# Optimization experiments

Hardware: AMD Instinct MI355X
Metric: run time of the kernel (lower is better)

The kernel has to match this reference:

```python
import jax, jax.numpy as jnp
import numpy as np

B, N_OBJ, OBJ_D = 256, 36, 2048
ATT_D, EMB_D, DEC_D, VOCAB, T = 1024, 1024, 1024, 10000, 20


def setup_inputs() -> dict:
    key = jax.random.key(0)
    ks = jax.random.split(key, 16)
    s = lambda *d: 1.0 / np.sqrt(d[-1])
    inp = {
        'encoder_out': jax.random.normal(ks[0], (B, EMB_D), jnp.float32),
        'objects': jax.random.normal(ks[1], (B, N_OBJ, OBJ_D), jnp.float32),
        'encoded_captions': jax.random.randint(ks[2], (B, T), 0, VOCAB),
        'caption_lengths': jax.random.randint(ks[3], (B, 1), 1, T + 1),
        'emb_table': jax.random.normal(ks[4], (VOCAB, EMB_D), jnp.float32) * 0.02,
        'W_enc_att': jax.random.normal(ks[5], (ATT_D, OBJ_D), jnp.float32) * s(OBJ_D),
        'b_enc_att': jnp.zeros((ATT_D,), jnp.float32),
        'W_dec_att': jax.random.normal(ks[6], (ATT_D, DEC_D), jnp.float32) * s(DEC_D),
        'b_dec_att': jnp.zeros((ATT_D,), jnp.float32),
        'w_full_att': jax.random.normal(ks[7], (1, ATT_D), jnp.float32) * s(ATT_D),
        'b_full_att': jnp.zeros((1,), jnp.float32),
        'W_fbeta': jax.random.normal(ks[8], (OBJ_D, DEC_D), jnp.float32) * s(DEC_D),
        'b_fbeta': jnp.zeros((OBJ_D,), jnp.float32),
        'W_ih': jax.random.normal(ks[9], (4 * DEC_D, EMB_D + OBJ_D), jnp.float32) * s(EMB_D + OBJ_D),
        'W_hh': jax.random.normal(ks[10], (4 * DEC_D, DEC_D), jnp.float32) * s(DEC_D),
        'b_ih': jnp.zeros((4 * DEC_D,), jnp.float32),
        'b_hh': jnp.zeros((4 * DEC_D,), jnp.float32),
        'W_fc': jax.random.normal(ks[11], (VOCAB, DEC_D), jnp.float32) * s(DEC_D),
        'b_fc': jnp.zeros((VOCAB,), jnp.float32),
    }
    return inp


def reference(encoder_out, objects, encoded_captions, caption_lengths,
              emb_table, W_enc_att, b_enc_att, W_dec_att, b_dec_att,
              w_full_att, b_full_att, W_fbeta, b_fbeta,
              W_ih, W_hh, b_ih, b_hh, W_fc, b_fc):
    lengths = caption_lengths[:, 0]
    sort_ind = jnp.argsort(-lengths)  # descending
    lengths = lengths[sort_ind]
    encoder_out = encoder_out[sort_ind]
    objects = objects[sort_ind]
    encoded_captions = encoded_captions[sort_ind]

    embeddings = emb_table[encoded_captions]  # (B, T, E)
    # step t input: encoder_out at t=0, embeddings[:, t-1] afterwards
    step_x = jnp.concatenate([encoder_out[:, None, :], embeddings[:, : T - 1, :]], axis=1)  # (B,T,E)

    att1 = jnp.einsum('bno,ao->bna', objects, W_enc_att) + b_enc_att  # (B,N,A), h-independent

    def step(carry, xs):
        h, c = carry
        x_t, t = xs  # (B,E), scalar
        active = (t < lengths)[:, None]  # (B,1) -- batch_size_t masking (lengths sorted desc)
        att2 = h @ W_dec_att.T + b_dec_att  # (B,A)
        e = (jax.nn.relu(att1 + att2[:, None, :]) @ w_full_att[0] + b_full_att[0])  # (B,N)
        alpha = jax.nn.softmax(e, axis=1)
        awe = jnp.einsum('bn,bno->bo', alpha, objects)  # (B,O)
        gate = jax.nn.sigmoid(h @ W_fbeta.T + b_fbeta)
        awe = gate * awe
        gates = jnp.concatenate([x_t, awe], axis=-1) @ W_ih.T + b_ih + h @ W_hh.T + b_hh
        i, f, g, o = jnp.split(gates, 4, axis=-1)  # torch LSTMCell order
        c_new = jax.nn.sigmoid(f) * c + jax.nn.sigmoid(i) * jnp.tanh(g)
        h_new = jax.nn.sigmoid(o) * jnp.tanh(c_new)
        h = jnp.where(active, h_new, h)
        c = jnp.where(active, c_new, c)
        preds = h_new @ W_fc.T + b_fc  # dropout in eval mode = identity
        preds = jnp.where(active, preds, 0.0)
        alpha = jnp.where(active, alpha, 0.0)
        return (h, c), (preds, alpha)

    h0 = jnp.zeros((B, DEC_D), objects.dtype)
    c0 = jnp.zeros((B, DEC_D), objects.dtype)
    xs = (jnp.swapaxes(step_x, 0, 1), jnp.arange(T))
    _, (preds, alphas) = jax.lax.scan(step, (h0, c0), xs)
    predictions = jnp.swapaxes(preds, 0, 1)  # (B,T,V)
    alphas = jnp.swapaxes(alphas, 0, 1)      # (B,T,N)
    return predictions, encoded_captions, lengths, alphas, sort_ind
```

## Files before the change

### kernel.cpp

```cpp
#include <hip/hip_runtime.h>
#include <hip/hip_bf16.h>
#include <cstdint>
#include <cstddef>

#define BB 256
#define TT 20
#define NOBJ 36
#define OBJD 2048
#define ATTD 1024
#define DECD 1024
#define VOCAB 10000
#define NBIG  17168
#define NBIGP 17216
#define NSPLIT 7168

typedef unsigned short u16;
typedef __attribute__((ext_vector_type(8))) short short8v;
typedef __attribute__((ext_vector_type(4))) float float4v;

__device__ inline u16 f2bf(float f) {
    __hip_bfloat16 h = __float2bfloat16(f);
    return *reinterpret_cast<u16*>(&h);
}
__device__ inline float bu(u16 u) {
    union { unsigned int i; float f; } x;
    x.i = ((unsigned int)u) << 16;
    return x.f;
}
__device__ inline float sigf(float x) { return 1.f / (1.f + expf(-x)); }

__global__ __launch_bounds__(256) void sort_kernel(
    const int* __restrict__ lens, int* __restrict__ sidx, int* __restrict__ slen,
    int* __restrict__ cnt, float* __restrict__ out_len, float* __restrict__ out_sind)
{
    __shared__ int L[BB];
    __shared__ int SL[BB];
    const int i = threadIdx.x;
    const int li = lens[i];
    L[i] = li;
    __syncthreads();
    int r = 0;
    for (int j = 0; j < BB; ++j) {
        const int lj = L[j];
        if (lj > li || (lj == li && j < i)) r++;
    }
    sidx[r] = i;
    slen[r] = li;
    SL[r] = li;
    out_sind[r] = (float)i;
    out_len[r]  = (float)li;
    __syncthreads();
    if (i < TT) {
        int cc = 0;
        for (int b = 0; b < BB; ++b) cc += (SL[b] > i);
        cnt[i] = cc;
    }
}

__global__ __launch_bounds__(256) void meta_kernel(
    const int* __restrict__ caps, const int* __restrict__ sidx,
    float* __restrict__ out_caps)
{
    const int idx = blockIdx.x * 256 + threadIdx.x;
    const int p = idx / TT, t = idx % TT;
    out_caps[idx] = (float)caps[sidx[p] * TT + t];
}

__global__ __launch_bounds__(256) void gather_objs(
    const float* __restrict__ objs, const int* __restrict__ sidx,
    u16* __restrict__ objsb)
{
    const int row = blockIdx.x;
    const int b = row / NOBJ, n = row - b * NOBJ;
    const float* src = objs + ((size_t)sidx[b] * NOBJ + n) * OBJD;
    u16* dst = objsb + (size_t)row * OBJD;
    const int tid = threadIdx.x;
    #pragma unroll
    for (int j = 0; j < 2; ++j) {
        float4 v = ((const float4*)src)[tid + 256 * j];
        ushort4 s;
        s.x = f2bf(v.x); s.y = f2bf(v.y); s.z = f2bf(v.z); s.w = f2bf(v.w);
        ((ushort4*)dst)[tid + 256 * j] = s;
    }
}

__global__ __launch_bounds__(256) void convWbig(
    const float* __restrict__ Wda, const float* __restrict__ bda,
    const float* __restrict__ Wfb, const float* __restrict__ bfb,
    const float* __restrict__ Whh,
    const float* __restrict__ Wfc, const float* __restrict__ bfc,
    u16* __restrict__ Wb, float* __restrict__ bcat)
{
    const int n = blockIdx.x;
    const int tid = threadIdx.x;
    const float* src = nullptr;
    float bb = 0.f;
    if (n < 1024)        { src = Wda + (size_t)n * 1024;            bb = bda[n]; }
    else if (n < 3072)   { src = Wfb + (size_t)(n - 1024) * 1024;   bb = bfb[n - 1024]; }
    else if (n < 7168)   { src = Whh + (size_t)(n - 3072) * 1024;   bb = 0.f; }
    else if (n < NBIG)   { src = Wfc + (size_t)(n - 7168) * 1024;   bb = bfc[n - 7168]; }
    u16* dst = Wb + (size_t)n * 1024;
    ushort4 s;
    if (src) {
        float4 v = ((const float4*)src)[tid];
        s.x = f2bf(v.x); s.y = f2bf(v.y); s.z = f2bf(v.z); s.w = f2bf(v.w);
    } else { s.x = s.y = s.z = s.w = 0; }
    ((ushort4*)dst)[tid] = s;
    if (tid == 0) bcat[n] = bb;
}

__global__ __launch_bounds__(256) void convWih(
    const float* __restrict__ Wih, const float* __restrict__ bih,
    const float* __restrict__ bhh, u16* __restrict__ Wb, float* __restrict__ bsum)
{
    const int n = blockIdx.x;
    const int tid = threadIdx.x;
    const float* src = Wih + (size_t)n * 3072;
    u16* dst = Wb + (size_t)n * 3072;
    #pragma unroll
    for (int j = 0; j < 3; ++j) {
        float4 v = ((const float4*)src)[tid + 256 * j];
        ushort4 s;
        s.x = f2bf(v.x); s.y = f2bf(v.y); s.z = f2bf(v.z); s.w = f2bf(v.w);
        ((ushort4*)dst)[tid + 256 * j] = s;
    }
    if (tid == 0) bsum[n] = bih[n] + bhh[n];
}

__global__ __launch_bounds__(256) void convWea(
    const float* __restrict__ Wea, u16* __restrict__ Wb)
{
    const int n = blockIdx.x;
    const int tid = threadIdx.x;
    const float* src = Wea + (size_t)n * OBJD;
    u16* dst = Wb + (size_t)n * OBJD;
    #pragma unroll
    for (int j = 0; j < 2; ++j) {
        float4 v = ((const float4*)src)[tid + 256 * j];
        ushort4 s;
        s.x = f2bf(v.x); s.y = f2bf(v.y); s.z = f2bf(v.z); s.w = f2bf(v.w);
        ((ushort4*)dst)[tid + 256 * j] = s;
    }
}

__global__ __launch_bounds__(256) void embed_kernel(
    const float* __restrict__ enc, const int* __restrict__ caps,
    const float* __restrict__ emb, const int* __restrict__ sidx,
    u16* __restrict__ Xb)
{
    const int blk = blockIdx.x;
    const int t = blk >> 8;
    const int b = blk & 255;
    const int sb = sidx[b];
    const float* src = (t == 0) ? (enc + (size_t)sb * DECD)
                                : (emb + (size_t)caps[sb * TT + (t - 1)] * DECD);
    const int tid = threadIdx.x;
    float4 v = ((const float4*)src)[tid];
    ushort4 s;
    s.x = f2bf(v.x); s.y = f2bf(v.y); s.z = f2bf(v.z); s.w = f2bf(v.w);
    ((ushort4*)(Xb + (size_t)blk * DECD))[tid] = s;
}

__global__ __launch_bounds__(256) void zero_hc(float* __restrict__ h, float* __restrict__ c)
{
    const int idx = blockIdx.x * 256 + threadIdx.x;
    if (idx < BB * DECD) h[idx] = 0.f;
    else                 c[idx - BB * DECD] = 0.f;
}

__global__ __launch_bounds__(256) void hcat0_kernel(
    const float* __restrict__ bcat, float* __restrict__ Hcat)
{
    const int col4 = blockIdx.x * 256 + threadIdx.x;
    const int m = blockIdx.y;
    ((float4*)(Hcat + (size_t)m * 7168))[col4] = ((const float4*)bcat)[col4];
}

template<int MF>
__global__ __launch_bounds__(256) void gemm_mfma(
    const u16* __restrict__ A, int lda,
    const u16* __restrict__ B, int ldb,
    const float* __restrict__ bias,
    float* __restrict__ C, u16* __restrict__ Cb, int ldc,
    int Nreal, int K,
    int nsplit, float* __restrict__ C2, int ldc2, const int* __restrict__ cntp)
{
    constexpr int BM = 64 * MF;
    constexpr int BK = 32;
    __shared__ u16 As[BM * BK];
    __shared__ u16 Bs[64 * BK];
    const int tid = threadIdx.x;
    const int lane = tid & 63;
    const int w = tid >> 6;
    const int m0 = blockIdx.y * BM;
    const int n0 = blockIdx.x * 64;

    float4v acc[MF][4];
    #pragma unroll
    for (int i = 0; i < MF; ++i)
        #pragma unroll
        for (int j = 0; j < 4; ++j) acc[i][j] = (float4v){0.f, 0.f, 0.f, 0.f};

    const int pa = tid * MF;
    const int ra = pa >> 2;
    const int fa = (ra >> 1) & 3;
    const int rb = tid >> 2;
    const int cbs = (tid & 3) ^ ((rb >> 1) & 3);
    const u16* Arow = A + (size_t)(m0 + ra) * lda;
    const u16* Brow = B + (size_t)(n0 + rb) * ldb;

    const int cfrag = lane >> 4;
    int slotA[MF], slotB[4];
    #pragma unroll
    for (int mi = 0; mi < MF; ++mi) {
        const int r = w * (16 * MF) + mi * 16 + (lane & 15);
        slotA[mi] = 4 * r + (cfrag ^ ((r >> 1) & 3));
    }
    #pragma unroll
    for (int nj = 0; nj < 4; ++nj) {
        const int rn = nj * 16 + (lane & 15);
        slotB[nj] = 4 * rn + (cfrag ^ ((rn >> 1) & 3));
    }

    for (int k0 = 0; k0 < K; k0 += BK) {
        short8v ast[MF];
        #pragma unroll
        for (int s = 0; s < MF; ++s) {
            const int c = ((pa + s) & 3) ^ fa;
            ast[s] = *(const short8v*)(Arow + k0 + c * 8);
        }
        short8v bst = *(const short8v*)(Brow + k0 + cbs * 8);
        __syncthreads();
        #pragma unroll
        for (int s = 0; s < MF; ++s)
            *(short8v*)&As[(pa + s) * 8] = ast[s];
        *(short8v*)&Bs[tid * 8] = bst;
        __syncthreads();

        short8v av[MF], bv[4];
        #pragma unroll
        for (int mi = 0; mi < MF; ++mi) av[mi] = *(const short8v*)&As[slotA[mi] * 8];
        #pragma unroll
        for (int nj = 0; nj < 4; ++nj) bv[nj] = *(const short8v*)&Bs[slotB[nj] * 8];
        #pragma unroll
        for (int mi = 0; mi < MF; ++mi)
            #pragma unroll
            for (int nj = 0; nj < 4; ++nj)
                acc[mi][nj] = __builtin_amdgcn_mfma_f32_16x16x32_bf16(
                    av[mi], bv[nj], acc[mi][nj], 0, 0, 0);
    }

    const int act = cntp ? *cntp : (1 << 30);
    #pragma unroll
    for (int mi = 0; mi < MF; ++mi) {
        const int mbase = m0 + w * (16 * MF) + mi * 16 + ((lane >> 4) << 2);
        #pragma unroll
        for (int nj = 0; nj < 4; ++nj) {
            const int n = n0 + nj * 16 + (lane & 15);
            if (n >= Nreal) continue;
            const float bval = bias[n];
            #pragma unroll
            for (int r = 0; r < 4; ++r) {
                const int m = mbase + r;
                const float v = acc[mi][nj][r] + bval;
                if (n < nsplit) {
                    if (Cb) Cb[(size_t)m * ldc + n] = f2bf(v);
                    else    C [(size_t)m * ldc + n] = v;
                } else {
                    C2[(size_t)m * ldc2 + (n - nsplit)] = (m < act) ? v : 0.f;
                }
            }
        }
    }
}

__global__ __launch_bounds__(256) void attn_kernel(
    const u16* __restrict__ att1b, const float* __restrict__ Hcat,
    const u16* __restrict__ objsb,
    const float* __restrict__ wfa, const float* __restrict__ bfa,
    const u16* __restrict__ Xb,
    const int* __restrict__ slen, int t,
    float* __restrict__ out_alph, u16* __restrict__ xcatb)
{
    __shared__ float wred[4][40];
    __shared__ float es[40];
    __shared__ float alph[40];
    const int b = blockIdx.x, tid = threadIdx.x;
    const int lane = tid & 63, w = tid >> 6;
    const float* hrow = Hcat + (size_t)b * 7168;
    const float4 h4 = ((const float4*)hrow)[tid];
    const float4 w4 = ((const float4*)wfa)[tid];
    const u16* a1base = att1b + (size_t)b * NOBJ * ATTD;

    float ep[NOBJ];
    #pragma unroll
    for (int n = 0; n < NOBJ; ++n) {
        ushort4 a4 = ((const ushort4*)(a1base + (size_t)n * ATTD))[tid];
        const float v0 = fmaxf(bu(a4.x) + h4.x, 0.f);
        const float v1 = fmaxf(bu(a4.y) + h4.y, 0.f);
        const float v2 = fmaxf(bu(a4.z) + h4.z, 0.f);
        const float v3 = fmaxf(bu(a4.w) + h4.w, 0.f);
        ep[n] = v0 * w4.x + v1 * w4.y + v2 * w4.z + v3 * w4.w;
    }
    #pragma unroll
    for (int n = 0; n < NOBJ; ++n) {
        float p = ep[n];
        #pragma unroll
        for (int off = 32; off > 0; off >>= 1) p += __shfl_down(p, off, 64);
        if (lane == 0) wred[w][n] = p;
    }
    __syncthreads();
    if (tid < NOBJ)
        es[tid] = wred[0][tid] + wred[1][tid] + wred[2][tid] + wred[3][tid] + bfa[0];
    __syncthreads();
    if (tid == 0) {
        float m = es[0];
        for (int n = 1; n < NOBJ; ++n) m = fmaxf(m, es[n]);
        float s = 0.f;
        for (int n = 0; n < NOBJ; ++n) { const float e = expf(es[n] - m); alph[n] = e; s += e; }
        const float inv = 1.f / s;
        for (int n = 0; n < NOBJ; ++n) alph[n] *= inv;
    }
    __syncthreads();
    const bool active = t < slen[b];
    if (tid < NOBJ)
        out_alph[((size_t)b * TT + t) * NOBJ + tid] = active ? alph[tid] : 0.f;

    float acc[8] = {0.f, 0.f, 0.f, 0.f, 0.f, 0.f, 0.f, 0.f};
    const u16* ob = objsb + (size_t)b * NOBJ * OBJD + tid * 8;
    #pragma unroll 4
    for (int n = 0; n < NOBJ; ++n) {
        const short8v ov = *(const short8v*)(ob + (size_t)n * OBJD);
        const float al = alph[n];
        #pragma unroll
        for (int j = 0; j < 8; ++j) acc[j] = fmaf(al, bu((u16)ov[j]), acc[j]);
    }
    const float* gp = hrow + 1024 + tid * 8;
    const float4 g0 = *(const float4*)gp;
    const float4 g1 = *(const float4*)(gp + 4);
    float gt[8] = {sigf(g0.x), sigf(g0.y), sigf(g0.z), sigf(g0.w),
                   sigf(g1.x), sigf(g1.y), sigf(g1.z), sigf(g1.w)};
    short8v st;
    #pragma unroll
    for (int j = 0; j < 8; ++j) st[j] = (short)f2bf(acc[j] * gt[j]);
    *(short8v*)&xcatb[(size_t)b * 3072 + 1024 + tid * 8] = st;

    ((ushort4*)(xcatb + (size_t)b * 3072))[tid] =
        ((const ushort4*)(Xb + ((size_t)t * BB + b) * DECD))[tid];
}

__global__ __launch_bounds__(256) void lstm_kernel(
    const float* __restrict__ G2, const float* __restrict__ Hcat,
    float* __restrict__ h, float* __restrict__ c, u16* __restrict__ hb,
    const int* __restrict__ slen, int t)
{
    const int idx = blockIdx.x * 256 + threadIdx.x;
    const int b = idx >> 8, d4 = idx & 255;
    const float4* g2 = (const float4*)(G2 + (size_t)b * 4096);
    const float4* hw = (const float4*)(Hcat + (size_t)b * 7168 + 3072);
    const float4 vi = g2[d4],       wi = hw[d4];
    const float4 vf = g2[256 + d4], wf = hw[256 + d4];
    const float4 vg = g2[512 + d4], wg = hw[512 + d4];
    const float4 vo = g2[768 + d4], wo = hw[768 + d4];
    float4* hp = (float4*)(h + (size_t)b * 1024);
    float4* cp = (float4*)(c + (size_t)b * 1024);
    const float4 hold = hp[d4];
    const float4 cold = cp[d4];
    float4 cn, hn;
    {
        const float si = sigf(vi.x + wi.x), sf = sigf(vf.x + wf.x), so = sigf(vo.x + wo.x);
        cn.x = sf * cold.x + si * tanhf(vg.x + wg.x); hn.x = so * tanhf(cn.x);
    }
    {
        const float si = sigf(vi.y + wi.y), sf = sigf(vf.y + wf.y), so = sigf(vo.y + wo.y);
        cn.y = sf * cold.y + si * tanhf(vg.y + wg.y); hn.y = so * tanhf(cn.y);
    }
    {
        const float si = sigf(vi.z + wi.z), sf = sigf(vf.z + wf.z), so = sigf(vo.z + wo.z);
        cn.z = sf * cold.z + si * tanhf(vg.z + wg.z); hn.z = so * tanhf(cn.z);
    }
    {
        const float si = sigf(vi.w + wi.w), sf = sigf(vf.w + wf.w), so = sigf(vo.w + wo.w);
        cn.w = sf * cold.w + si * tanhf(vg.w + wg.w); hn.w = so * tanhf(cn.w);
    }
    const bool active = t < slen[b];
    const float4 hcur = active ? hn : hold;
    if (active) { hp[d4] = hn; cp[d4] = cn; }
    ushort4 s;
    s.x = f2bf(hcur.x); s.y = f2bf(hcur.y); s.z = f2bf(hcur.z); s.w = f2bf(hcur.w);
    ((ushort4*)(hb + (size_t)b * 1024))[d4] = s;
}

extern "C" void kernel_launch(void* const* d_in, const int* in_sizes, int n_in,
                              void* d_out, int out_size, void* d_ws, size_t ws_size,
                              hipStream_t stream)
{
    const float* enc  = (const float*)d_in[0];
    const float* objs = (const float*)d_in[1];
    const int*   caps = (const int*)d_in[2];
    const int*   clen = (const int*)d_in[3];
    const float* emb  = (const float*)d_in[4];
    const float* Wea  = (const float*)d_in[5];
    const float* bea  = (const float*)d_in[6];
    const float* Wda  = (const float*)d_in[7];
    const float* bda  = (const float*)d_in[8];
    const float* wfa  = (const float*)d_in[9];
    const float* bfa  = (const float*)d_in[10];
    const float* Wfb  = (const float*)d_in[11];
    const float* bfb  = (const float*)d_in[12];
    const float* Wih  = (const float*)d_in[13];
    const float* Whh  = (const float*)d_in[14];
    const float* bih  = (const float*)d_in[15];
    const float* bhh  = (const float*)d_in[16];
    const float* Wfc  = (const float*)d_in[17];
    const float* bfc  = (const float*)d_in[18];

    float* outP     = (float*)d_out;
    float* out_caps = outP + (size_t)BB * TT * VOCAB;
    float* out_len  = out_caps + BB * TT;
    float* out_alph = out_len + BB;
    float* out_sind = out_alph + (size_t)BB * TT * NOBJ;

    char* wp = (char*)d_ws;
    auto alloc = [&](size_t bytes) -> void* {
        void* r = (void*)wp;
        wp += (bytes + 255) & ~(size_t)255;
        return r;
    };
    int*   sidx  = (int*)alloc(BB * 4);
    int*   slen  = (int*)alloc(BB * 4);
    int*   cnt   = (int*)alloc(32 * 4);
    u16*   objsb = (u16*)alloc((size_t)BB * NOBJ * OBJD * 2);
    u16*   Wbigb = (u16*)alloc((size_t)NBIGP * 1024 * 2);
    float* bcat  = (float*)alloc(NBIGP * 4);
    u16*   Wihb  = (u16*)alloc((size_t)4096 * 3072 * 2);
    float* bsum  = (float*)alloc(4096 * 4);
    u16*   Weab  = (u16*)alloc((size_t)1024 * OBJD * 2);
    u16*   att1b = (u16*)alloc((size_t)BB * NOBJ * ATTD * 2);
    u16*   Xb    = (u16*)alloc((size_t)TT * BB * DECD * 2);
    float* Hcat  = (float*)alloc((size_t)BB * 7168 * 4);
    u16*   xcatb = (u16*)alloc((size_t)BB * 3072 * 2);
    float* G2    = (float*)alloc((size_t)BB * 4096 * 4);
    float* h     = (float*)alloc((size_t)BB * DECD * 4);
    float* c     = (float*)alloc((size_t)BB * DECD * 4);
    u16*   hb    = (u16*)alloc((size_t)BB * DECD * 2);
    (void)ws_size; (void)in_sizes; (void)n_in; (void)out_size;

    sort_kernel<<<1, 256, 0, stream>>>(clen, sidx, slen, cnt, out_len, out_sind);
    meta_kernel<<<20, 256, 0, stream>>>(caps, sidx, out_caps);
    gather_objs<<<BB * NOBJ, 256, 0, stream>>>(objs, sidx, objsb);
    convWbig<<<NBIGP, 256, 0, stream>>>(Wda, bda, Wfb, bfb, Whh, Wfc, bfc, Wbigb, bcat);
    convWih<<<4096, 256, 0, stream>>>(Wih, bih, bhh, Wihb, bsum);
    convWea<<<1024, 256, 0, stream>>>(Wea, Weab);
    embed_kernel<<<TT * BB, 256, 0, stream>>>(enc, caps, emb, sidx, Xb);
    zero_hc<<<2048, 256, 0, stream>>>(h, c);
    hcat0_kernel<<<dim3(7, 256), 256, 0, stream>>>(bcat, Hcat);

    gemm_mfma<2><<<dim3(16, 72), 256, 0, stream>>>(
        objsb, OBJD, Weab, OBJD, bea, nullptr, att1b, ATTD,
        ATTD, OBJD, 1 << 30, nullptr, 0, nullptr);

    for (int t = 0; t < TT; ++t) {
        attn_kernel<<<BB, 256, 0, stream>>>(att1b, Hcat, objsb, wfa, bfa, Xb,
                                            slen, t, out_alph, xcatb);
        gemm_mfma<1><<<dim3(64, 4), 256, 0, stream>>>(
            xcatb, 3072, Wihb, 3072, bsum, G2, nullptr, 4096,
            4096, 3072, 1 << 30, nullptr, 0, nullptr);
        lstm_kernel<<<256, 256, 0, stream>>>(G2, Hcat, h, c, hb, slen, t);
        gemm_mfma<2><<<dim3(NBIGP / 64, 2), 256, 0, stream>>>(
            hb, DECD, Wbigb, DECD, bcat, Hcat, nullptr, 7168,
            NBIG, DECD, NSPLIT, outP + (size_t)t * VOCAB, TT * VOCAB, cnt + t);
    }
}
```

Baseline: 1.994 ms.

## Hoist embedding gate GEMM out of the loop, add 128x128 LDS-DMA GEMM and row skipping

Computes the embedding half of the LSTM input projection for all timesteps in one large GEMM before the recurrence. Inside the loop, only the attention-weighted half (K=2048) remains, run as a split-K GEMM whose four partial sums are added in the LSTM kernel. A new 128x128-tile GEMM loads operands with global_load_lds directly into LDS and skips row tiles beyond the active caption count. The attention and LSTM kernels exit early for finished sequences, and attention is split over two blocks per batch row. The cost is extra memory for the precomputed gates and partial-sum traffic, plus larger tiles that leave fewer blocks for the small per-step GEMMs.

```diff
diff --git a/kernel.cpp b/kernel.cpp
--- a/kernel.cpp
+++ b/kernel.cpp
@@ -11,7 +11,7 @@
 #define DECD 1024
 #define VOCAB 10000
 #define NBIG  17168
-#define NBIGP 17216
+#define NBIGP 17280
 #define NSPLIT 7168
 
 typedef unsigned short u16;
@@ -28,6 +28,12 @@
     return x.f;
 }
 __device__ inline float sigf(float x) { return 1.f / (1.f + expf(-x)); }
+
+__device__ inline void gload16(const u16* g, u16* l) {
+    __builtin_amdgcn_global_load_lds(
+        (const __attribute__((address_space(1))) unsigned int*)g,
+        (__attribute__((address_space(3))) unsigned int*)l, 16, 0, 0);
+}
 
 __global__ __launch_bounds__(256) void sort_kernel(
     const int* __restrict__ lens, int* __restrict__ sidx, int* __restrict__ slen,
@@ -176,96 +182,98 @@
     ((float4*)(Hcat + (size_t)m * 7168))[col4] = ((const float4*)bcat)[col4];
 }
 
-template<int MF>
-__global__ __launch_bounds__(256) void gemm_mfma(
+__global__ __launch_bounds__(256) void gemm128(
     const u16* __restrict__ A, int lda,
     const u16* __restrict__ B, int ldb,
     const float* __restrict__ bias,
-    float* __restrict__ C, u16* __restrict__ Cb, int ldc,
-    int Nreal, int K,
+    float* __restrict__ Cf, u16* __restrict__ Cb, int ldc,
+    int Nreal, int kzlen, size_t zCstride,
     int nsplit, float* __restrict__ C2, int ldc2, const int* __restrict__ cntp)
 {
-    constexpr int BM = 64 * MF;
-    constexpr int BK = 32;
-    __shared__ u16 As[BM * BK];
-    __shared__ u16 Bs[64 * BK];
+    __shared__ u16 As[128 * 32];
+    __shared__ u16 Bs[128 * 32];
     const int tid = threadIdx.x;
     const int lane = tid & 63;
     const int w = tid >> 6;
-    const int m0 = blockIdx.y * BM;
-    const int n0 = blockIdx.x * 64;
-
-    float4v acc[MF][4];
-    #pragma unroll
-    for (int i = 0; i < MF; ++i)
+    const int wr = w >> 1, wc = w & 1;
+    const int m0 = blockIdx.y * 128;
+    const int n0 = blockIdx.x * 128;
+    const int kbase = blockIdx.z * kzlen;
+    A += kbase;
+    B += kbase;
+    if (Cf) Cf += (size_t)blockIdx.z * zCstride;
+
+    const int act = cntp ? *cntp : (1 << 30);
+    float4v acc[4][4];
+    #pragma unroll
+    for (int i = 0; i < 4; ++i)
         #pragma unroll
         for (int j = 0; j < 4; ++j) acc[i][j] = (float4v){0.f, 0.f, 0.f, 0.f};
 
-    const int pa = tid * MF;
-    const int ra = pa >> 2;
-    const int fa = (ra >> 1) & 3;
-    const int rb = tid >> 2;
-    const int cbs = (tid & 3) ^ ((rb >> 1) & 3);
-    const u16* Arow = A + (size_t)(m0 + ra) * lda;
-    const u16* Brow = B + (size_t)(n0 + rb) * ldb;
-
-    const int cfrag = lane >> 4;
-    int slotA[MF], slotB[4];
-    #pragma unroll
-    for (int mi = 0; mi < MF; ++mi) {
-        const int r = w * (16 * MF) + mi * 16 + (lane & 15);
-        slotA[mi] = 4 * r + (cfrag ^ ((r >> 1) & 3));
-    }
-    #pragma unroll
-    for (int nj = 0; nj < 4; ++nj) {
-        const int rn = nj * 16 + (lane & 15);
-        slotB[nj] = 4 * rn + (cfrag ^ ((rn >> 1) & 3));
-    }
-
-    for (int k0 = 0; k0 < K; k0 += BK) {
-        short8v ast[MF];
+    if (m0 < act) {
+        const int r0 = (w * 2 + 0) * 16 + (lane >> 2);
+        const int r1 = (w * 2 + 1) * 16 + (lane >> 2);
+        const int s0 = (lane & 3) ^ ((r0 >> 1) & 3);
+        const int s1 = (lane & 3) ^ ((r1 >> 1) & 3);
+        const u16* gA0 = A + (size_t)(m0 + r0) * lda + s0 * 8;
+        const u16* gA1 = A + (size_t)(m0 + r1) * lda + s1 * 8;
+        const u16* gB0 = B + (size_t)(n0 + r0) * ldb + s0 * 8;
+        const u16* gB1 = B + (size_t)(n0 + r1) * ldb + s1 * 8;
+        u16* lA0 = &As[(w * 2 + 0) * 16 * 32];
+        u16* lA1 = &As[(w * 2 + 1) * 16 * 32];
+        u16* lB0 = &Bs[(w * 2 + 0) * 16 * 32];
+        u16* lB1 = &Bs[(w * 2 + 1) * 16 * 32];
+
+        int ia[4], ib[4];
         #pragma unroll
-        for (int s = 0; s < MF; ++s) {
-            const int c = ((pa + s) & 3) ^ fa;
-            ast[s] = *(const short8v*)(Arow + k0 + c * 8);
+        for (int mi = 0; mi < 4; ++mi) {
+            const int r = wr * 64 + mi * 16 + (lane & 15);
+            ia[mi] = r * 32 + (((lane >> 4) ^ ((r >> 1) & 3)) << 3);
         }
-        short8v bst = *(const short8v*)(Brow + k0 + cbs * 8);
-        __syncthreads();
-        #pragma unroll
-        for (int s = 0; s < MF; ++s)
-            *(short8v*)&As[(pa + s) * 8] = ast[s];
-        *(short8v*)&Bs[tid * 8] = bst;
-        __syncthreads();
-
-        short8v av[MF], bv[4];
-        #pragma unroll
-        for (int mi = 0; mi < MF; ++mi) av[mi] = *(const short8v*)&As[slotA[mi] * 8];
-        #pragma unroll
-        for (int nj = 0; nj < 4; ++nj) bv[nj] = *(const short8v*)&Bs[slotB[nj] * 8];
-        #pragma unroll
-        for (int mi = 0; mi < MF; ++mi)
-            #pragma unroll
-            for (int nj = 0; nj < 4; ++nj)
-                acc[mi][nj] = __builtin_amdgcn_mfma_f32_16x16x32_bf16(
-                    av[mi], bv[nj], acc[mi][nj], 0, 0, 0);
-    }
-
-    const int act = cntp ? *cntp : (1 << 30);
-    #pragma unroll
-    for (int mi = 0; mi < MF; ++mi) {
-        const int mbase = m0 + w * (16 * MF) + mi * 16 + ((lane >> 4) << 2);
         #pragma unroll
         for (int nj = 0; nj < 4; ++nj) {
-            const int n = n0 + nj * 16 + (lane & 15);
+            const int r = wc * 64 + nj * 16 + (lane & 15);
+            ib[nj] = r * 32 + (((lane >> 4) ^ ((r >> 1) & 3)) << 3);
+        }
+
+        const int nk = kzlen >> 5;
+        for (int it = 0; it < nk; ++it) {
+            gload16(gA0, lA0);
+            gload16(gA1, lA1);
+            gload16(gB0, lB0);
+            gload16(gB1, lB1);
+            gA0 += 32; gA1 += 32; gB0 += 32; gB1 += 32;
+            __syncthreads();
+            short8v av[4], bv[4];
+            #pragma unroll
+            for (int mi = 0; mi < 4; ++mi) av[mi] = *(const short8v*)&As[ia[mi]];
+            #pragma unroll
+            for (int nj = 0; nj < 4; ++nj) bv[nj] = *(const short8v*)&Bs[ib[nj]];
+            #pragma unroll
+            for (int mi = 0; mi < 4; ++mi)
+                #pragma unroll
+                for (int nj = 0; nj < 4; ++nj)
+                    acc[mi][nj] = __builtin_amdgcn_mfma_f32_16x16x32_bf16(
+                        av[mi], bv[nj], acc[mi][nj], 0, 0, 0);
+            __syncthreads();
+        }
+    }
+
+    #pragma unroll
+    for (int mi = 0; mi < 4; ++mi) {
+        const int mbase = m0 + wr * 64 + mi * 16 + ((lane >> 4) << 2);
+        #pragma unroll
+        for (int nj = 0; nj < 4; ++nj) {
+            const int n = n0 + wc * 64 + nj * 16 + (lane & 15);
             if (n >= Nreal) continue;
-            const float bval = bias[n];
+            const float bval = bias ? bias[n] : 0.f;
             #pragma unroll
             for (int r = 0; r < 4; ++r) {
                 const int m = mbase + r;
                 const float v = acc[mi][nj][r] + bval;
                 if (n < nsplit) {
                     if (Cb) Cb[(size_t)m * ldc + n] = f2bf(v);
-                    else    C [(size_t)m * ldc + n] = v;
+                    else    Cf[(size_t)m * ldc + n] = v;
                 } else {
                     C2[(size_t)m * ldc2 + (n - nsplit)] = (m < act) ? v : 0.f;
                 }
@@ -278,14 +286,19 @@
     const u16* __restrict__ att1b, const float* __restrict__ Hcat,
     const u16* __restrict__ objsb,
     const float* __restrict__ wfa, const float* __restrict__ bfa,
-    const u16* __restrict__ Xb,
     const int* __restrict__ slen, int t,
-    float* __restrict__ out_alph, u16* __restrict__ xcatb)
-{
+    float* __restrict__ out_alph, u16* __restrict__ aweb)
+{
+    const int b = blockIdx.x, z = blockIdx.y, tid = threadIdx.x;
+    const bool active = t < slen[b];
+    if (!active) {
+        if (z == 0 && tid < NOBJ)
+            out_alph[((size_t)b * TT + t) * NOBJ + tid] = 0.f;
+        return;
+    }
     __shared__ float wred[4][40];
     __shared__ float es[40];
     __shared__ float alph[40];
-    const int b = blockIdx.x, tid = threadIdx.x;
     const int lane = tid & 63, w = tid >> 6;
     const float* hrow = Hcat + (size_t)b * 7168;
     const float4 h4 = ((const float4*)hrow)[tid];
@@ -322,72 +335,80 @@
         for (int n = 0; n < NOBJ; ++n) alph[n] *= inv;
     }
     __syncthreads();
-    const bool active = t < slen[b];
-    if (tid < NOBJ)
-        out_alph[((size_t)b * TT + t) * NOBJ + tid] = active ? alph[tid] : 0.f;
-
-    float acc[8] = {0.f, 0.f, 0.f, 0.f, 0.f, 0.f, 0.f, 0.f};
-    const u16* ob = objsb + (size_t)b * NOBJ * OBJD + tid * 8;
+    if (z == 0 && tid < NOBJ)
+        out_alph[((size_t)b * TT + t) * NOBJ + tid] = alph[tid];
+
+    float acc[4] = {0.f, 0.f, 0.f, 0.f};
+    const u16* ob = objsb + (size_t)b * NOBJ * OBJD + z * 1024 + tid * 4;
     #pragma unroll 4
     for (int n = 0; n < NOBJ; ++n) {
-        const short8v ov = *(const short8v*)(ob + (size_t)n * OBJD);
+        const ushort4 ov = *(const ushort4*)(ob + (size_t)n * OBJD);
         const float al = alph[n];
-        #pragma unroll
-        for (int j = 0; j < 8; ++j) acc[j] = fmaf(al, bu((u16)ov[j]), acc[j]);
-    }
-    const float* gp = hrow + 1024 + tid * 8;
-    const float4 g0 = *(const float4*)gp;
-    const float4 g1 = *(const float4*)(gp + 4);
-    float gt[8] = {sigf(g0.x), sigf(g0.y), sigf(g0.z), sigf(g0.w),
-                   sigf(g1.x), sigf(g1.y), sigf(g1.z), sigf(g1.w)};
-    short8v st;
-    #pragma unroll
-    for (int j = 0; j < 8; ++j) st[j] = (short)f2bf(acc[j] * gt[j]);
-    *(short8v*)&xcatb[(size_t)b * 3072 + 1024 + tid * 8] = st;
-
-    ((ushort4*)(xcatb + (size_t)b * 3072))[tid] =
-        ((const ushort4*)(Xb + ((size_t)t * BB + b) * DECD))[tid];
+        acc[0] = fmaf(al, bu(ov.x), acc[0]);
+        acc[1] = fmaf(al, bu(ov.y), acc[1]);
+        acc[2] = fmaf(al, bu(ov.z), acc[2]);
+        acc[3] = fmaf(al, bu(ov.w), acc[3]);
+    }
+    const float4 g0 = *(const float4*)(hrow + 1024 + z * 1024 + tid * 4);
+    ushort4 st;
+    st.x = f2bf(acc[0] * sigf(g0.x));
+    st.y = f2bf(acc[1] * sigf(g0.y));
+    st.z = f2bf(acc[2] * sigf(g0.z));
+    st.w = f2bf(acc[3] * sigf(g0.w));
+    *(ushort4*)&aweb[(size_t)b * 2048 + z * 1024 + tid * 4] = st;
 }
 
 __global__ __launch_bounds__(256) void lstm_kernel(
-    const float* __restrict__ G2, const float* __restrict__ Hcat,
+    const float* __restrict__ G2p, const u16* __restrict__ Gxb,
+    const float* __restrict__ Hcat,
     float* __restrict__ h, float* __restrict__ c, u16* __restrict__ hb,
     const int* __restrict__ slen, int t)
 {
     const int idx = blockIdx.x * 256 + threadIdx.x;
     const int b = idx >> 8, d4 = idx & 255;
-    const float4* g2 = (const float4*)(G2 + (size_t)b * 4096);
-    const float4* hw = (const float4*)(Hcat + (size_t)b * 7168 + 3072);
-    const float4 vi = g2[d4],       wi = hw[d4];
-    const float4 vf = g2[256 + d4], wf = hw[256 + d4];
-    const float4 vg = g2[512 + d4], wg = hw[512 + d4];
-    const float4 vo = g2[768 + d4], wo = hw[768 + d4];
+    if (t >= slen[b]) return;
+    const float4* pw = (const float4*)(Hcat + (size_t)b * 7168 + 3072);
+    const u16* gx = Gxb + ((size_t)(t * BB + b)) * 4096;
+
+    float4 g[4];
+    #pragma unroll
+    for (int q = 0; q < 4; ++q) {
+        const ushort4 xv = ((const ushort4*)(gx + q * 1024))[d4];
+        float4 s;
+        s.x = bu(xv.x); s.y = bu(xv.y); s.z = bu(xv.z); s.w = bu(xv.w);
+        const float4 hv = pw[q * 256 + d4];
+        s.x += hv.x; s.y += hv.y; s.z += hv.z; s.w += hv.w;
+        #pragma unroll
+        for (int p = 0; p < 4; ++p) {
+            const float4 pv = ((const float4*)G2p)[(size_t)p * (BB * 1024) + b * 1024 + q * 256 + d4];
+            s.x += pv.x; s.y += pv.y; s.z += pv.z; s.w += pv.w;
+        }
+        g[q] = s;
+    }
     float4* hp = (float4*)(h + (size_t)b * 1024);
     float4* cp = (float4*)(c + (size_t)b * 1024);
-    const float4 hold = hp[d4];
     const float4 cold = cp[d4];
     float4 cn, hn;
     {
-        const float si = sigf(vi.x + wi.x), sf = sigf(vf.x + wf.x), so = sigf(vo.x + wo.x);
-        cn.x = sf * cold.x + si * tanhf(vg.x + wg.x); hn.x = so * tanhf(cn.x);
+        const float si = sigf(g[0].x), sf = sigf(g[1].x), so = sigf(g[3].x);
+        cn.x = sf * cold.x + si * tanhf(g[2].x); hn.x = so * tanhf(cn.x);
     }
     {
-        const float si = sigf(vi.y + wi.y), sf = sigf(vf.y + wf.y), so = sigf(vo.y + wo.y);
-        cn.y = sf * cold.y + si * tanhf(vg.y + wg.y); hn.y = so * tanhf(cn.y);
+        const float si = sigf(g[0].y), sf = sigf(g[1].y), so = sigf(g[3].y);
+        cn.y = sf * cold.y + si * tanhf(g[2].y); hn.y = so * tanhf(cn.y);
     }
     {
-        const float si = sigf(vi.z + wi.z), sf = sigf(vf.z + wf.z), so = sigf(vo.z + wo.z);
-        cn.z = sf * cold.z + si * tanhf(vg.z + wg.z); hn.z = so * tanhf(cn.z);
+        const float si = sigf(g[0].z), sf = sigf(g[1].z), so = sigf(g[3].z);
+        cn.z = sf * cold.z + si * tanhf(g[2].z); hn.z = so * tanhf(cn.z);
     }
     {
-        const float si = sigf(vi.w + wi.w), sf = sigf(vf.w + wf.w), so = sigf(vo.w + wo.w);
-        cn.w = sf * cold.w + si * tanhf(vg.w + wg.w); hn.w = so * tanhf(cn.w);
-    }
-    const bool active = t < slen[b];
-    const float4 hcur = active ? hn : hold;
-    if (active) { hp[d4] = hn; cp[d4] = cn; }
+        const float si = sigf(g[0].w), sf = sigf(g[1].w), so = sigf(g[3].w);
+        cn.w = sf * cold.w + si * tanhf(g[2].w); hn.w = so * tanhf(cn.w);
+    }
+    hp[d4] = hn;
+    cp[d4] = cn;
     ushort4 s;
-    s.x = f2bf(hcur.x); s.y = f2bf(hcur.y); s.z = f2bf(hcur.z); s.w = f2bf(hcur.w);
+    s.x = f2bf(hn.x); s.y = f2bf(hn.y); s.z = f2bf(hn.z); s.w = f2bf(hn.w);
     ((ushort4*)(hb + (size_t)b * 1024))[d4] = s;
 }
 
@@ -438,9 +459,10 @@
     u16*   Weab  = (u16*)alloc((size_t)1024 * OBJD * 2);
     u16*   att1b = (u16*)alloc((size_t)BB * NOBJ * ATTD * 2);
     u16*   Xb    = (u16*)alloc((size_t)TT * BB * DECD * 2);
+    u16*   Gxb   = (u16*)alloc((size_t)TT * BB * 4096 * 2);
     float* Hcat  = (float*)alloc((size_t)BB * 7168 * 4);
-    u16*   xcatb = (u16*)alloc((size_t)BB * 3072 * 2);
-    float* G2    = (float*)alloc((size_t)BB * 4096 * 4);
+    u16*   aweb  = (u16*)alloc((size_t)BB * 2048 * 2);
+    float* G2p   = (float*)alloc((size_t)4 * BB * 4096 * 4);
     float* h     = (float*)alloc((size_t)BB * DECD * 4);
     float* c     = (float*)alloc((size_t)BB * DECD * 4);
     u16*   hb    = (u16*)alloc((size_t)BB * DECD * 2);
@@ -456,19 +478,23 @@
     zero_hc<<<2048, 256, 0, stream>>>(h, c);
     hcat0_kernel<<<dim3(7, 256), 256, 0, stream>>>(bcat, Hcat);
 
-    gemm_mfma<2><<<dim3(16, 72), 256, 0, stream>>>(
+    gemm128<<<dim3(8, 72, 1), 256, 0, stream>>>(
         objsb, OBJD, Weab, OBJD, bea, nullptr, att1b, ATTD,
-        ATTD, OBJD, 1 << 30, nullptr, 0, nullptr);
+        ATTD, OBJD, 0, 1 << 30, nullptr, 0, nullptr);
+
+    gemm128<<<dim3(32, 40, 1), 256, 0, stream>>>(
+        Xb, DECD, Wihb, 3072, bsum, nullptr, Gxb, 4096,
+        4096, DECD, 0, 1 << 30, nullptr, 0, nullptr);
 
     for (int t = 0; t < TT; ++t) {
-        attn_kernel<<<BB, 256, 0, stream>>>(att1b, Hcat, objsb, wfa, bfa, Xb,
-                                            slen, t, out_alph, xcatb);
-        gemm_mfma<1><<<dim3(64, 4), 256, 0, stream>>>(
-            xcatb, 3072, Wihb, 3072, bsum, G2, nullptr, 4096,
-            4096, 3072, 1 << 30, nullptr, 0, nullptr);
-        lstm_kernel<<<256, 256, 0, stream>>>(G2, Hcat, h, c, hb, slen, t);
-        gemm_mfma<2><<<dim3(NBIGP / 64, 2), 256, 0, stream>>>(
+        attn_kernel<<<dim3(BB, 2), 256, 0, stream>>>(
+            att1b, Hcat, objsb, wfa, bfa, slen, t, out_alph, aweb);
+        gemm128<<<dim3(32, 2, 4), 256, 0, stream>>>(
+            aweb, 2048, Wihb + 1024, 3072, nullptr, G2p, nullptr, 4096,
+            4096, 512, (size_t)BB * 4096, 1 << 30, nullptr, 0, cnt + t);
+        lstm_kernel<<<256, 256, 0, stream>>>(G2p, Gxb, Hcat, h, c, hb, slen, t);
+        gemm128<<<dim3(NBIGP / 128, 2, 1), 256, 0, stream>>>(
             hb, DECD, Wbigb, DECD, bcat, Hcat, nullptr, 7168,
-            NBIG, DECD, NSPLIT, outP + (size_t)t * VOCAB, TT * VOCAB, cnt + t);
-    }
-}
+            NBIG, DECD, 0, NSPLIT, outP + (size_t)t * VOCAB, TT * VOCAB, cnt + t);
+    }
+}
```

Result: faster. 1.872 ms (-6.1%).
